# Optimization experiments

Measured on AMD Instinct MI355X. Metric: run time of the kernel, lower is better.

## Reference

```python
import jax, jax.numpy as jnp
import numpy as np

B, N_UNITS, SEQ, H = 4, 1024, 2048, 8
D_HEAD = N_UNITS // H
SCALE = 1.0 / D_HEAD ** 0.5


def setup_inputs() -> dict:
    key = jax.random.key(0)
    k1, k2, k3 = jax.random.split(key, 3)
    x = jax.random.normal(k1, (B, N_UNITS, SEQ), dtype=jnp.float32)
    # conv1x1 weights, bias=False; scaled like typical init
    W_qkv = jax.random.normal(k2, (3 * N_UNITS, N_UNITS), dtype=jnp.float32) * (1.0 / N_UNITS ** 0.5)
    W_out = jax.random.normal(k3, (N_UNITS, N_UNITS), dtype=jnp.float32) * (1.0 / N_UNITS ** 0.5)
    return {"x": x, "W_qkv": W_qkv, "W_out": W_out}


def reference(x, W_qkv, W_out):
    # x: (B, n_units, S). Conv1x1 == per-position linear along channel dim.
    qkv = jnp.einsum('oc,bcs->bos', W_qkv, x)          # (B, 3*n_units, S)
    Q, K, V = jnp.split(qkv, 3, axis=1)                # each (B, n_units, S)
    # torch.chunk along channels into h heads == reshape (B, h, d_head, S)
    Q = Q.reshape(B, H, D_HEAD, SEQ)
    K = K.reshape(B, H, D_HEAD, SEQ)
    V = V.reshape(B, H, D_HEAD, SEQ)
    # scores: Q^T K * scale  (NO softmax in original module; mask unused)
    A = jnp.einsum('bhdq,bhdk->bhqk', Q, K) * SCALE    # (B, h, S, S)
    # aggregation: sum_k A[q,k] * V[d,k]  (original does broadcast mul+sum)
    C = jnp.einsum('bhqk,bhdk->bhdq', A, V)            # (B, h, d_head, S)
    C = C.reshape(B, N_UNITS, SEQ)
    out = jnp.einsum('oc,bcs->bos', W_out, C)          # (B, n_units, S)
    return out
```

## Files before the change

kernel.cpp:

```cpp
#include <hip/hip_runtime.h>
#include <hip/hip_bf16.h>
#include <stdint.h>

using bf16 = __hip_bfloat16;

typedef __bf16 bf16x8 __attribute__((ext_vector_type(8)));
typedef float  f32x4  __attribute__((ext_vector_type(4)));

constexpr int Bc = 4, Hh = 8, Dh = 128, S = 2048, Cn = 1024, O3 = 3072;
constexpr float SCALE = 0.08838834764831845f;

#define GLDS16(gp, lp)                                               \
  __builtin_amdgcn_global_load_lds(                                  \
      (const __attribute__((address_space(1))) void*)(gp),           \
      (__attribute__((address_space(3))) void*)(lp), 16, 0, 0)

#define WAITVM(N) asm volatile("s_waitcnt vmcnt(" #N ")" ::: "memory")
#define BAR()                                  \
  do {                                         \
    asm volatile("" ::: "memory");             \
    __builtin_amdgcn_s_barrier();              \
    asm volatile("" ::: "memory");             \
  } while (0)

__device__ __forceinline__ void gemm_bt_core(
    const bf16* __restrict__ Abase, int lda,
    const bf16* __restrict__ Bbase, int ldb,
    int kIters, f32x4 (&acc)[4][4])
{
  alignas(16) __shared__ bf16 As[128 * 32];
  alignas(16) __shared__ bf16 Bs[128 * 32];
  const int t    = threadIdx.x;
  const int lane = t & 63;
  const int quad = lane >> 4, r16 = lane & 15;
  const int wave = t >> 6;
  const int wm = (wave & 1) * 64, wn = (wave >> 1) * 64;
  const int lrow = lane >> 2;
  const int lk   = (lane & 3) * 8;

  const long aOff0 = (long)(wave * 32 + lrow) * lda + lk;
  const long aOff1 = aOff0 + 16l * lda;
  const long bOff0 = (long)(wave * 32 + lrow) * ldb + lk;
  const long bOff1 = bOff0 + 16l * ldb;
  bf16* aL0 = &As[(wave * 32) * 32];
  bf16* aL1 = &As[(wave * 32 + 16) * 32];
  bf16* bL0 = &Bs[(wave * 32) * 32];
  bf16* bL1 = &Bs[(wave * 32 + 16) * 32];

#pragma unroll
  for (int i = 0; i < 4; i++)
#pragma unroll
    for (int j = 0; j < 4; j++) acc[i][j] = {0.f, 0.f, 0.f, 0.f};

  for (int ks = 0; ks < kIters; ++ks) {
    const int k0 = ks * 32;
    __syncthreads();
    GLDS16(Abase + k0 + aOff0, aL0);
    GLDS16(Abase + k0 + aOff1, aL1);
    GLDS16(Bbase + k0 + bOff0, bL0);
    GLDS16(Bbase + k0 + bOff1, bL1);
    __syncthreads();
    bf16x8 af[4], bfr[4];
#pragma unroll
    for (int i = 0; i < 4; i++)
      af[i] = *(const bf16x8*)&As[(wm + i * 16 + r16) * 32 + quad * 8];
#pragma unroll
    for (int j = 0; j < 4; j++)
      bfr[j] = *(const bf16x8*)&Bs[(wn + j * 16 + r16) * 32 + quad * 8];
#pragma unroll
    for (int i = 0; i < 4; i++)
#pragma unroll
      for (int j = 0; j < 4; j++)
        acc[i][j] = __builtin_amdgcn_mfma_f32_16x16x32_bf16(af[i], bfr[j], acc[i][j], 0, 0, 0);
  }
}

__device__ __forceinline__ void store_bf16_tile(
    f32x4 (&acc)[4][4], bf16* __restrict__ Cp, int ldc)
{
  const int t = threadIdx.x;
  const int lane = t & 63;
  const int quad = lane >> 4, r16 = lane & 15;
  const int wave = t >> 6;
  const int wm = (wave & 1) * 64, wn = (wave >> 1) * 64;
#pragma unroll
  for (int i = 0; i < 4; i++)
#pragma unroll
    for (int j = 0; j < 4; j++)
#pragma unroll
      for (int r = 0; r < 4; r++) {
        const int row = wm + i * 16 + quad * 4 + r;
        const int col = wn + j * 16 + r16;
        Cp[(long)row * ldc + col] = __float2bfloat16(acc[i][j][r]);
      }
}

__device__ __forceinline__ void store_f32_tile(
    f32x4 (&acc)[4][4], float* __restrict__ Cp, int ldc)
{
  const int t = threadIdx.x;
  const int lane = t & 63;
  const int quad = lane >> 4, r16 = lane & 15;
  const int wave = t >> 6;
  const int wm = (wave & 1) * 64, wn = (wave >> 1) * 64;
#pragma unroll
  for (int i = 0; i < 4; i++)
#pragma unroll
    for (int j = 0; j < 4; j++)
#pragma unroll
      for (int r = 0; r < 4; r++) {
        const int row = wm + i * 16 + quad * 4 + r;
        const int col = wn + j * 16 + r16;
        Cp[(long)row * ldc + col] = acc[i][j][r];
      }
}

__global__ __launch_bounds__(512, 2) void k_gemm_kv8(
    const bf16* __restrict__ WkvB, const bf16* __restrict__ xT, bf16* __restrict__ KV)
{
  constexpr int NT = Cn / 32;
  alignas(16) __shared__ bf16 smem[4 * 16384];

  const int orig = blockIdx.x;
  const int mt = orig >> 5;
  const int nt = ((orig & 7) << 2) | ((orig >> 3) & 3);
  const int m0 = mt * 256;

  const int tid  = threadIdx.x;
  const int lane = tid & 63;
  const int w    = tid >> 6;
  const int quad = lane >> 4, r16 = lane & 15;
  const int wm = (w >> 2) * 128;
  const int wn = (w & 3) * 64;

  const int srow = w * 16 + (lane >> 2);
  const int cx   = (lane & 3) ^ ((lane >> 3) & 3);
  const bf16* Ag = WkvB + (long)(m0 + srow) * Cn + cx * 8;
  const bf16* Bg = xT + (long)((long)nt * 256 + srow) * Cn + cx * 8;
  const int ldsW = w * 512;

#define KV8_STAGE_A(tt)                                                   \
  do {                                                                    \
    const int k0_ = (tt) * 32, bb_ = ((tt) & 3) * 16384;                  \
    GLDS16(Ag + k0_,             &smem[bb_ + ldsW]);                      \
    GLDS16(Ag + 128l * Cn + k0_, &smem[bb_ + 4096 + ldsW]);               \
  } while (0)
#define KV8_STAGE_B(tt)                                                   \
  do {                                                                    \
    const int k0_ = (tt) * 32, bb_ = ((tt) & 3) * 16384;                  \
    GLDS16(Bg + k0_,             &smem[bb_ + 8192 + ldsW]);               \
    GLDS16(Bg + 128l * Cn + k0_, &smem[bb_ + 8192 + 4096 + ldsW]);        \
  } while (0)

  const int sc8 = (quad ^ ((r16 >> 1) & 3)) * 8;

  f32x4 acc[8][4];
#pragma unroll
  for (int m = 0; m < 8; m++)
#pragma unroll
    for (int n = 0; n < 4; n++) acc[m][n] = {0.f, 0.f, 0.f, 0.f};

  KV8_STAGE_A(0); KV8_STAGE_B(0);
  KV8_STAGE_A(1); KV8_STAGE_B(1);
  KV8_STAGE_A(2); KV8_STAGE_B(2);
  WAITVM(8);
  BAR();

  bf16x8 af0[4], bfr0[4], af1[4];
  {
    const bf16* Ab = &smem[0];
    const bf16* Bb = Ab + 8192;
#pragma unroll
    for (int n = 0; n < 4; n++)
      bfr0[n] = *(const bf16x8*)&Bb[(wn + n * 16 + r16) * 32 + sc8];
#pragma unroll
    for (int m = 0; m < 4; m++)
      af0[m] = *(const bf16x8*)&Ab[(wm + m * 16 + r16) * 32 + sc8];
  }

#pragma unroll 4
  for (int tt = 0; tt < NT; ++tt) {
    const bf16* Ab = &smem[(tt & 3) * 16384];

    BAR();
    if (tt + 3 < NT) { KV8_STAGE_A(tt + 3); KV8_STAGE_B(tt + 3); }
#pragma unroll
    for (int m = 0; m < 4; m++)
      af1[m] = *(const bf16x8*)&Ab[(wm + (m + 4) * 16 + r16) * 32 + sc8];
    __builtin_amdgcn_s_setprio(1);
#pragma unroll
    for (int m = 0; m < 4; m++)
#pragma unroll
      for (int n = 0; n < 4; n++)
        acc[m][n] = __builtin_amdgcn_mfma_f32_16x16x32_bf16(af0[m], bfr0[n], acc[m][n], 0, 0, 0);
    __builtin_amdgcn_s_setprio(0);

    if (tt <= NT - 4)      { WAITVM(8); }
    else if (tt == NT - 3) { WAITVM(4); }
    else if (tt == NT - 2) { WAITVM(0); }
    BAR();

    __builtin_amdgcn_s_setprio(1);
#pragma unroll
    for (int m = 0; m < 4; m++)
#pragma unroll
      for (int n = 0; n < 4; n++)
        acc[m + 4][n] = __builtin_amdgcn_mfma_f32_16x16x32_bf16(af1[m], bfr0[n], acc[m + 4][n], 0, 0, 0);
    __builtin_amdgcn_s_setprio(0);

    if (tt + 1 < NT) {
      const bf16* Ab2 = &smem[((tt + 1) & 3) * 16384];
      const bf16* Bb2 = Ab2 + 8192;
#pragma unroll
      for (int n = 0; n < 4; n++)
        bfr0[n] = *(const bf16x8*)&Bb2[(wn + n * 16 + r16) * 32 + sc8];
#pragma unroll
      for (int m = 0; m < 4; m++)
        af0[m] = *(const bf16x8*)&Ab2[(wm + m * 16 + r16) * 32 + sc8];
    }
  }

  bf16* Cp = KV + (long)(nt >> 3) * 2048 * S + (long)m0 * S + (nt & 7) * 256;
#pragma unroll
  for (int m = 0; m < 8; m++)
#pragma unroll
    for (int n = 0; n < 4; n++)
#pragma unroll
      for (int r = 0; r < 4; r++) {
        const int row = wm + m * 16 + quad * 4 + r;
        const int col = wn + n * 16 + r16;
        Cp[(long)row * S + col] = __float2bfloat16(acc[m][n][r]);
      }
#undef KV8_STAGE_A
#undef KV8_STAGE_B
}

__global__ __launch_bounds__(512, 2) void k_gemm_out8(
    const bf16* __restrict__ W2, const bf16* __restrict__ QT, float* __restrict__ out)
{
  constexpr int NT = Cn / 32;
  alignas(16) __shared__ bf16 smem[4 * 12288];

  const int orig = blockIdx.x;
  const int swz  = (orig & 7) * 32 + (orig >> 3);
  const int b  = swz >> 6;
  const int mt = (swz >> 3) & 7;
  const int nt = swz & 7;
  const int m0 = mt * 128, n0 = nt * 256;

  const int tid  = threadIdx.x;
  const int lane = tid & 63;
  const int w    = tid >> 6;
  const int quad = lane >> 4, r16 = lane & 15;
  const int wm = (w >> 2) * 64;
  const int wn = (w & 3) * 64;

  const int srow = w * 16 + (lane >> 2);
  const int cx   = (lane & 3) ^ ((lane >> 3) & 3);
  const bf16* Ag = W2 + (long)b * Cn * Cn + (long)(m0 + srow) * Cn + cx * 8;
  const bf16* Bg = QT + (long)b * S * Cn + (long)(n0 + srow) * Cn + cx * 8;
  const int ldsW = w * 512;

#define OUT_STAGE(tt)                                                     \
  do {                                                                    \
    const int k0_ = (tt) * 32, bb_ = ((tt) & 3) * 12288;                  \
    GLDS16(Ag + k0_,             &smem[bb_ + ldsW]);                      \
    GLDS16(Bg + k0_,             &smem[bb_ + 4096 + ldsW]);               \
    GLDS16(Bg + 128l * Cn + k0_, &smem[bb_ + 8192 + ldsW]);               \
  } while (0)

  const int sc8 = (quad ^ ((r16 >> 1) & 3)) * 8;

  f32x4 acc[4][4];
#pragma unroll
  for (int m = 0; m < 4; m++)
#pragma unroll
    for (int n = 0; n < 4; n++) acc[m][n] = {0.f, 0.f, 0.f, 0.f};

  OUT_STAGE(0); OUT_STAGE(1); OUT_STAGE(2);
  WAITVM(6);
  BAR();

  bf16x8 af0[2], bfr0[4], af1[2];
  {
    const bf16* Ab = &smem[0];
    const bf16* Bb = Ab + 4096;
#pragma unroll
    for (int n = 0; n < 4; n++)
      bfr0[n] = *(const bf16x8*)&Bb[(wn + n * 16 + r16) * 32 + sc8];
#pragma unroll
    for (int m = 0; m < 2; m++)
      af0[m] = *(const bf16x8*)&Ab[(wm + m * 16 + r16) * 32 + sc8];
  }

#pragma unroll 4
  for (int tt = 0; tt < NT; ++tt) {
    const bf16* Ab = &smem[(tt & 3) * 12288];

    BAR();
    if (tt + 3 < NT) OUT_STAGE(tt + 3);
#pragma unroll
    for (int m = 0; m < 2; m++)
      af1[m] = *(const bf16x8*)&Ab[(wm + (m + 2) * 16 + r16) * 32 + sc8];
    __builtin_amdgcn_s_setprio(1);
#pragma unroll
    for (int m = 0; m < 2; m++)
#pragma unroll
      for (int n = 0; n < 4; n++)
        acc[m][n] = __builtin_amdgcn_mfma_f32_16x16x32_bf16(af0[m], bfr0[n], acc[m][n], 0, 0, 0);
    __builtin_amdgcn_s_setprio(0);

    if (tt <= NT - 4)      { WAITVM(6); }
    else if (tt == NT - 3) { WAITVM(3); }
    else if (tt == NT - 2) { WAITVM(0); }
    BAR();

    __builtin_amdgcn_s_setprio(1);
#pragma unroll
    for (int m = 0; m < 2; m++)
#pragma unroll
      for (int n = 0; n < 4; n++)
        acc[m + 2][n] = __builtin_amdgcn_mfma_f32_16x16x32_bf16(af1[m], bfr0[n], acc[m + 2][n], 0, 0, 0);
    __builtin_amdgcn_s_setprio(0);

    if (tt + 1 < NT) {
      const bf16* Ab2 = &smem[((tt + 1) & 3) * 12288];
      const bf16* Bb2 = Ab2 + 4096;
#pragma unroll
      for (int n = 0; n < 4; n++)
        bfr0[n] = *(const bf16x8*)&Bb2[(wn + n * 16 + r16) * 32 + sc8];
#pragma unroll
      for (int m = 0; m < 2; m++)
        af0[m] = *(const bf16x8*)&Ab2[(wm + m * 16 + r16) * 32 + sc8];
    }
  }

  float* Cp = out + (long)b * Cn * S + (long)m0 * S + n0;
#pragma unroll
  for (int m = 0; m < 4; m++)
#pragma unroll
    for (int n = 0; n < 4; n++)
#pragma unroll
      for (int r = 0; r < 4; r++) {
        const int row = wm + m * 16 + quad * 4 + r;
        const int col = wn + n * 16 + r16;
        Cp[(long)row * S + col] = acc[m][n][r];
      }
#undef OUT_STAGE
}

__global__ __launch_bounds__(512, 2) void k_gemm_qt8(
    const bf16* __restrict__ xT, const bf16* __restrict__ WqB, bf16* __restrict__ QT)
{
  constexpr int NT = Cn / 32;
  alignas(16) __shared__ bf16 smem[4 * 12288];

  const int orig = blockIdx.x;
  const int b  = orig >> 6;
  const int mt = (orig >> 2) & 15;
  const int nt = orig & 3;
  const int m0 = mt * 128, n0 = nt * 256;

  const int tid  = threadIdx.x;
  const int lane = tid & 63;
  const int w    = tid >> 6;
  const int quad = lane >> 4, r16 = lane & 15;
  const int wm = (w >> 2) * 64;
  const int wn = (w & 3) * 64;

  const int srow = w * 16 + (lane >> 2);
  const int cx   = (lane & 3) ^ ((lane >> 3) & 3);
  const bf16* Ag = xT + (long)b * S * Cn + (long)(m0 + srow) * Cn + cx * 8;
  const bf16* Bg = WqB + (long)(n0 + srow) * Cn + cx * 8;
  const int ldsW = w * 512;

#define QT_STAGE(tt)                                                      \
  do {                                                                    \
    const int k0_ = (tt) * 32, bb_ = ((tt) & 3) * 12288;                  \
    GLDS16(Ag + k0_,             &smem[bb_ + ldsW]);                      \
    GLDS16(Bg + k0_,             &smem[bb_ + 4096 + ldsW]);               \
    GLDS16(Bg + 128l * Cn + k0_, &smem[bb_ + 8192 + ldsW]);               \
  } while (0)

  const int sc8 = (quad ^ ((r16 >> 1) & 3)) * 8;

  f32x4 acc[4][4];
#pragma unroll
  for (int m = 0; m < 4; m++)
#pragma unroll
    for (int n = 0; n < 4; n++) acc[m][n] = {0.f, 0.f, 0.f, 0.f};

  QT_STAGE(0); QT_STAGE(1); QT_STAGE(2);
  WAITVM(6);
  BAR();

  bf16x8 af0[2], bfr0[4], af1[2];
  {
    const bf16* Ab = &smem[0];
    const bf16* Bb = Ab + 4096;
#pragma unroll
    for (int n = 0; n < 4; n++)
      bfr0[n] = *(const bf16x8*)&Bb[(wn + n * 16 + r16) * 32 + sc8];
#pragma unroll
    for (int m = 0; m < 2; m++)
      af0[m] = *(const bf16x8*)&Ab[(wm + m * 16 + r16) * 32 + sc8];
  }

#pragma unroll 4
  for (int tt = 0; tt < NT; ++tt) {
    const bf16* Ab = &smem[(tt & 3) * 12288];

    BAR();
    if (tt + 3 < NT) QT_STAGE(tt + 3);
#pragma unroll
    for (int m = 0; m < 2; m++)
      af1[m] = *(const bf16x8*)&Ab[(wm + (m + 2) * 16 + r16) * 32 + sc8];
    __builtin_amdgcn_s_setprio(1);
#pragma unroll
    for (int m = 0; m < 2; m++)
#pragma unroll
      for (int n = 0; n < 4; n++)
        acc[m][n] = __builtin_amdgcn_mfma_f32_16x16x32_bf16(af0[m], bfr0[n], acc[m][n], 0, 0, 0);
    __builtin_amdgcn_s_setprio(0);

    if (tt <= NT - 4)      { WAITVM(6); }
    else if (tt == NT - 3) { WAITVM(3); }
    else if (tt == NT - 2) { WAITVM(0); }
    BAR();

    __builtin_amdgcn_s_setprio(1);
#pragma unroll
    for (int m = 0; m < 2; m++)
#pragma unroll
      for (int n = 0; n < 4; n++)
        acc[m + 2][n] = __builtin_amdgcn_mfma_f32_16x16x32_bf16(af1[m], bfr0[n], acc[m + 2][n], 0, 0, 0);
    __builtin_amdgcn_s_setprio(0);

    if (tt + 1 < NT) {
      const bf16* Ab2 = &smem[((tt + 1) & 3) * 12288];
      const bf16* Bb2 = Ab2 + 4096;
#pragma unroll
      for (int n = 0; n < 4; n++)
        bfr0[n] = *(const bf16x8*)&Bb2[(wn + n * 16 + r16) * 32 + sc8];
#pragma unroll
      for (int m = 0; m < 2; m++)
        af0[m] = *(const bf16x8*)&Ab2[(wm + m * 16 + r16) * 32 + sc8];
    }
  }

  bf16* Cp = QT + (long)b * S * Cn + (long)m0 * Cn + n0;
#pragma unroll
  for (int m = 0; m < 4; m++)
#pragma unroll
    for (int n = 0; n < 4; n++)
#pragma unroll
      for (int r = 0; r < 4; r++) {
        const int row = wm + m * 16 + quad * 4 + r;
        const int col = wn + n * 16 + r16;
        Cp[(long)row * Cn + col] = __float2bfloat16(acc[m][n][r]);
      }
#undef QT_STAGE
}

__global__ __launch_bounds__(256) void k_cvt_w(
    const float* __restrict__ Wqkv, const float* __restrict__ Wout,
    bf16* __restrict__ WqkvB, bf16* __restrict__ WoutB)
{
  const long v = (long)blockIdx.x * 256 + threadIdx.x;
  const bool isQ = v < 786432;
  const float4 f = isQ ? ((const float4*)Wqkv)[v] : ((const float4*)Wout)[v - 786432];
  bf16 tmp[4];
  tmp[0] = __float2bfloat16(f.x);
  tmp[1] = __float2bfloat16(f.y);
  tmp[2] = __float2bfloat16(f.z);
  tmp[3] = __float2bfloat16(f.w);
  ushort4 u = *(ushort4*)tmp;
  if (isQ) ((ushort4*)WqkvB)[v] = u;
  else     ((ushort4*)WoutB)[v - 786432] = u;
}

__global__ __launch_bounds__(256) void k_transpose_cvt(
    const float* __restrict__ in, bf16* __restrict__ out, long inZ, long outZ)
{
  __shared__ bf16 tile[32][33];
  const float* ip = in + (long)blockIdx.z * inZ;
  bf16* op = out + (long)blockIdx.z * outZ;
  const int c0 = blockIdx.x * 32, r0 = blockIdx.y * 32;
  const int tx = threadIdx.x & 31, ty = threadIdx.x >> 5;
#pragma unroll
  for (int i = 0; i < 32; i += 8)
    tile[ty + i][tx] = __float2bfloat16(ip[(long)(r0 + ty + i) * 2048 + c0 + tx]);
  __syncthreads();
#pragma unroll
  for (int i = 0; i < 32; i += 8)
    op[(long)(c0 + ty + i) * 1024 + r0 + tx] = tile[tx][ty + i];
}

__global__ __launch_bounds__(256) void k_gemm_mt(
    const bf16* __restrict__ KV, float* __restrict__ MTpart)
{
  const int chunk = blockIdx.x;
  const int z = blockIdx.y;
  const int b = z >> 3, h = z & 7;
  const bf16* base = KV + (long)b * 2048 * S;
  const bf16* A  = base + (long)(h * Dh) * S + chunk * 256;
  const bf16* Bp = base + (long)(1024 + h * Dh) * S + chunk * 256;
  f32x4 acc[4][4];
  gemm_bt_core(A, S, Bp, S, 8, acc);
  store_f32_tile(acc, MTpart + ((long)chunk * 32 + z) * (Dh * Dh), Dh);
}

__global__ __launch_bounds__(256) void k_reduce_mt(
    const float* __restrict__ MTpart, bf16* __restrict__ MbT)
{
  const long i = (long)blockIdx.x * 256 + threadIdx.x;
  float s = 0.f;
#pragma unroll
  for (int c = 0; c < 8; c++) s += MTpart[(long)c * 32 * Dh * Dh + i];
  MbT[i] = __float2bfloat16(s * SCALE);
}

__global__ __launch_bounds__(256) void k_gemm_w2(
    const bf16* __restrict__ WoutB, const bf16* __restrict__ MbT, bf16* __restrict__ W2)
{
  const int m0 = blockIdx.x * 128;
  const int h = blockIdx.y, b = blockIdx.z;
  const int z = b * 8 + h;
  f32x4 acc[4][4];
  gemm_bt_core(WoutB + (long)m0 * Cn + h * Dh, Cn,
               MbT + (long)z * Dh * Dh, Dh, 4, acc);
  store_bf16_tile(acc, W2 + (long)b * Cn * Cn + (long)m0 * Cn + h * Dh, Cn);
}

extern "C" void kernel_launch(void* const* d_in, const int* in_sizes, int n_in,
                              void* d_out, int out_size, void* d_ws, size_t ws_size,
                              hipStream_t stream)
{
  const float* x    = (const float*)d_in[0];
  const float* Wqkv = (const float*)d_in[1];
  const float* Wout = (const float*)d_in[2];
  float* out = (float*)d_out;

  char* ws = (char*)d_ws;
  bf16*  KV     = (bf16*)ws;
  bf16*  xT     = (bf16*)(ws + 33554432);
  float* MTpart = (float*)(ws + 50331648);
  bf16*  QT     = (bf16*)(ws + 50331648);
  bf16*  WqkvB  = (bf16*)(ws + 67108864);
  bf16*  WoutB  = (bf16*)(ws + 73400320);
  bf16*  MbT    = (bf16*)(ws + 75497472);
  bf16*  W2     = (bf16*)(ws + 76546048);
  bf16*  WkvB   = WqkvB + (long)Cn * Cn;

  k_cvt_w<<<dim3(4096), 256, 0, stream>>>(Wqkv, Wout, WqkvB, WoutB);
  k_transpose_cvt<<<dim3(64, 32, 4), 256, 0, stream>>>(
      x, xT, (long)1024 * 2048, (long)2048 * 1024);
  k_gemm_kv8<<<dim3(256), 512, 0, stream>>>(WkvB, xT, KV);
  k_gemm_mt<<<dim3(8, 32), 256, 0, stream>>>(KV, MTpart);
  k_reduce_mt<<<dim3(2048), 256, 0, stream>>>(MTpart, MbT);
  k_gemm_w2<<<dim3(8, 8, 4), 256, 0, stream>>>(WoutB, MbT, W2);
  k_gemm_qt8<<<dim3(256), 512, 0, stream>>>(xT, WqkvB, QT);
  k_gemm_out8<<<dim3(256), 512, 0, stream>>>(W2, QT, out);
}
```

Baseline: 197.8 us.

## Merge KV and QT projection GEMMs into one launch and fuse prep kernels

The KV and Q^T projection GEMMs become device functions dispatched by block index inside one 512-block kernel, so both run concurrently and fill the GPU together. The weight conversion and the x transpose-convert kernels are merged into a single prep launch. MTpart scratch now lives in the output buffer, which is free until the final GEMM overwrites it. The cost is shared LDS sized for the larger KV body in both branches and a less balanced mix of block workloads.

```diff
diff --git a/kernel.cpp b/kernel.cpp
--- a/kernel.cpp
+++ b/kernel.cpp
@@ -115,13 +115,11 @@
       }
 }
 
-__global__ __launch_bounds__(512, 2) void k_gemm_kv8(
-    const bf16* __restrict__ WkvB, const bf16* __restrict__ xT, bf16* __restrict__ KV)
+__device__ __forceinline__ void kv_body(
+    const bf16* __restrict__ WkvB, const bf16* __restrict__ xT,
+    bf16* __restrict__ KV, bf16* sm, int orig)
 {
   constexpr int NT = Cn / 32;
-  alignas(16) __shared__ bf16 smem[4 * 16384];
-
-  const int orig = blockIdx.x;
   const int mt = orig >> 5;
   const int nt = ((orig & 7) << 2) | ((orig >> 3) & 3);
   const int m0 = mt * 256;
@@ -142,14 +140,14 @@
 #define KV8_STAGE_A(tt)                                                   \
   do {                                                                    \
     const int k0_ = (tt) * 32, bb_ = ((tt) & 3) * 16384;                  \
-    GLDS16(Ag + k0_,             &smem[bb_ + ldsW]);                      \
-    GLDS16(Ag + 128l * Cn + k0_, &smem[bb_ + 4096 + ldsW]);               \
+    GLDS16(Ag + k0_,             &sm[bb_ + ldsW]);                        \
+    GLDS16(Ag + 128l * Cn + k0_, &sm[bb_ + 4096 + ldsW]);                 \
   } while (0)
 #define KV8_STAGE_B(tt)                                                   \
   do {                                                                    \
     const int k0_ = (tt) * 32, bb_ = ((tt) & 3) * 16384;                  \
-    GLDS16(Bg + k0_,             &smem[bb_ + 8192 + ldsW]);               \
-    GLDS16(Bg + 128l * Cn + k0_, &smem[bb_ + 8192 + 4096 + ldsW]);        \
+    GLDS16(Bg + k0_,             &sm[bb_ + 8192 + ldsW]);                 \
+    GLDS16(Bg + 128l * Cn + k0_, &sm[bb_ + 8192 + 4096 + ldsW]);          \
   } while (0)
 
   const int sc8 = (quad ^ ((r16 >> 1) & 3)) * 8;
@@ -168,7 +166,7 @@
 
   bf16x8 af0[4], bfr0[4], af1[4];
   {
-    const bf16* Ab = &smem[0];
+    const bf16* Ab = &sm[0];
     const bf16* Bb = Ab + 8192;
 #pragma unroll
     for (int n = 0; n < 4; n++)
@@ -180,7 +178,7 @@
 
 #pragma unroll 4
   for (int tt = 0; tt < NT; ++tt) {
-    const bf16* Ab = &smem[(tt & 3) * 16384];
+    const bf16* Ab = &sm[(tt & 3) * 16384];
 
     BAR();
     if (tt + 3 < NT) { KV8_STAGE_A(tt + 3); KV8_STAGE_B(tt + 3); }
@@ -209,7 +207,7 @@
     __builtin_amdgcn_s_setprio(0);
 
     if (tt + 1 < NT) {
-      const bf16* Ab2 = &smem[((tt + 1) & 3) * 16384];
+      const bf16* Ab2 = &sm[((tt + 1) & 3) * 16384];
       const bf16* Bb2 = Ab2 + 8192;
 #pragma unroll
       for (int n = 0; n < 4; n++)
@@ -235,6 +233,164 @@
 #undef KV8_STAGE_B
 }
 
+__device__ __forceinline__ void qt_body(
+    const bf16* __restrict__ xT, const bf16* __restrict__ WqB,
+    bf16* __restrict__ QT, bf16* sm, int orig)
+{
+  constexpr int NT = Cn / 32;
+  const int b  = orig >> 6;
+  const int mt = (orig >> 2) & 15;
+  const int nt = orig & 3;
+  const int m0 = mt * 128, n0 = nt * 256;
+
+  const int tid  = threadIdx.x;
+  const int lane = tid & 63;
+  const int w    = tid >> 6;
+  const int quad = lane >> 4, r16 = lane & 15;
+  const int wm = (w >> 2) * 64;
+  const int wn = (w & 3) * 64;
+
+  const int srow = w * 16 + (lane >> 2);
+  const int cx   = (lane & 3) ^ ((lane >> 3) & 3);
+  const bf16* Ag = xT + (long)b * S * Cn + (long)(m0 + srow) * Cn + cx * 8;
+  const bf16* Bg = WqB + (long)(n0 + srow) * Cn + cx * 8;
+  const int ldsW = w * 512;
+
+#define QT_STAGE(tt)                                                      \
+  do {                                                                    \
+    const int k0_ = (tt) * 32, bb_ = ((tt) & 3) * 12288;                  \
+    GLDS16(Ag + k0_,             &sm[bb_ + ldsW]);                        \
+    GLDS16(Bg + k0_,             &sm[bb_ + 4096 + ldsW]);                 \
+    GLDS16(Bg + 128l * Cn + k0_, &sm[bb_ + 8192 + ldsW]);                 \
+  } while (0)
+
+  const int sc8 = (quad ^ ((r16 >> 1) & 3)) * 8;
+
+  f32x4 acc[4][4];
+#pragma unroll
+  for (int m = 0; m < 4; m++)
+#pragma unroll
+    for (int n = 0; n < 4; n++) acc[m][n] = {0.f, 0.f, 0.f, 0.f};
+
+  QT_STAGE(0); QT_STAGE(1); QT_STAGE(2);
+  WAITVM(6);
+  BAR();
+
+  bf16x8 af0[2], bfr0[4], af1[2];
+  {
+    const bf16* Ab = &sm[0];
+    const bf16* Bb = Ab + 4096;
+#pragma unroll
+    for (int n = 0; n < 4; n++)
+      bfr0[n] = *(const bf16x8*)&Bb[(wn + n * 16 + r16) * 32 + sc8];
+#pragma unroll
+    for (int m = 0; m < 2; m++)
+      af0[m] = *(const bf16x8*)&Ab[(wm + m * 16 + r16) * 32 + sc8];
+  }
+
+#pragma unroll 4
+  for (int tt = 0; tt < NT; ++tt) {
+    const bf16* Ab = &sm[(tt & 3) * 12288];
+
+    BAR();
+    if (tt + 3 < NT) QT_STAGE(tt + 3);
+#pragma unroll
+    for (int m = 0; m < 2; m++)
+      af1[m] = *(const bf16x8*)&Ab[(wm + (m + 2) * 16 + r16) * 32 + sc8];
+    __builtin_amdgcn_s_setprio(1);
+#pragma unroll
+    for (int m = 0; m < 2; m++)
+#pragma unroll
+      for (int n = 0; n < 4; n++)
+        acc[m][n] = __builtin_amdgcn_mfma_f32_16x16x32_bf16(af0[m], bfr0[n], acc[m][n], 0, 0, 0);
+    __builtin_amdgcn_s_setprio(0);
+
+    if (tt <= NT - 4)      { WAITVM(6); }
+    else if (tt == NT - 3) { WAITVM(3); }
+    else if (tt == NT - 2) { WAITVM(0); }
+    BAR();
+
+    __builtin_amdgcn_s_setprio(1);
+#pragma unroll
+    for (int m = 0; m < 2; m++)
+#pragma unroll
+      for (int n = 0; n < 4; n++)
+        acc[m + 2][n] = __builtin_amdgcn_mfma_f32_16x16x32_bf16(af1[m], bfr0[n], acc[m + 2][n], 0, 0, 0);
+    __builtin_amdgcn_s_setprio(0);
+
+    if (tt + 1 < NT) {
+      const bf16* Ab2 = &sm[((tt + 1) & 3) * 12288];
+      const bf16* Bb2 = Ab2 + 4096;
+#pragma unroll
+      for (int n = 0; n < 4; n++)
+        bfr0[n] = *(const bf16x8*)&Bb2[(wn + n * 16 + r16) * 32 + sc8];
+#pragma unroll
+      for (int m = 0; m < 2; m++)
+        af0[m] = *(const bf16x8*)&Ab2[(wm + m * 16 + r16) * 32 + sc8];
+    }
+  }
+
+  bf16* Cp = QT + (long)b * S * Cn + (long)m0 * Cn + n0;
+#pragma unroll
+  for (int m = 0; m < 4; m++)
+#pragma unroll
+    for (int n = 0; n < 4; n++)
+#pragma unroll
+      for (int r = 0; r < 4; r++) {
+        const int row = wm + m * 16 + quad * 4 + r;
+        const int col = wn + n * 16 + r16;
+        Cp[(long)row * Cn + col] = __float2bfloat16(acc[m][n][r]);
+      }
+#undef QT_STAGE
+}
+
+__global__ __launch_bounds__(512, 2) void k_kvqt8(
+    const bf16* __restrict__ WkvB, const bf16* __restrict__ xT,
+    bf16* __restrict__ KV, const bf16* __restrict__ WqB, bf16* __restrict__ QT)
+{
+  alignas(16) __shared__ bf16 smem[4 * 16384];
+  const int bid = blockIdx.x;
+  if (bid < 256) kv_body(WkvB, xT, KV, smem, bid);
+  else           qt_body(xT, WqB, QT, smem, bid - 256);
+}
+
+__global__ __launch_bounds__(256) void k_prep(
+    const float* __restrict__ x, bf16* __restrict__ xT,
+    const float* __restrict__ Wqkv, const float* __restrict__ Wout,
+    bf16* __restrict__ WqkvB, bf16* __restrict__ WoutB)
+{
+  __shared__ bf16 tile[32][33];
+  if (blockIdx.z < 4) {
+    const float* ip = x + (long)blockIdx.z * 1024 * 2048;
+    bf16* op = xT + (long)blockIdx.z * 2048 * 1024;
+    const int c0 = blockIdx.x * 32, r0 = blockIdx.y * 32;
+    const int tx = threadIdx.x & 31, ty = threadIdx.x >> 5;
+#pragma unroll
+    for (int i = 0; i < 32; i += 8)
+      tile[ty + i][tx] = __float2bfloat16(ip[(long)(r0 + ty + i) * 2048 + c0 + tx]);
+    __syncthreads();
+#pragma unroll
+    for (int i = 0; i < 32; i += 8)
+      op[(long)(c0 + ty + i) * 1024 + r0 + tx] = tile[tx][ty + i];
+  } else {
+    const long blk = (long)blockIdx.x + (long)blockIdx.y * 64;
+#pragma unroll
+    for (int i = 0; i < 2; i++) {
+      const long v = blk * 512 + i * 256 + threadIdx.x;
+      const bool isQ = v < 786432;
+      const float4 f = isQ ? ((const float4*)Wqkv)[v] : ((const float4*)Wout)[v - 786432];
+      bf16 tmp[4];
+      tmp[0] = __float2bfloat16(f.x);
+      tmp[1] = __float2bfloat16(f.y);
+      tmp[2] = __float2bfloat16(f.z);
+      tmp[3] = __float2bfloat16(f.w);
+      ushort4 u = *(ushort4*)tmp;
+      if (isQ) ((ushort4*)WqkvB)[v] = u;
+      else     ((ushort4*)WoutB)[v - 786432] = u;
+    }
+  }
+}
+
 __global__ __launch_bounds__(512, 2) void k_gemm_out8(
     const bf16* __restrict__ W2, const bf16* __restrict__ QT, float* __restrict__ out)
 {
@@ -347,153 +503,6 @@
         Cp[(long)row * S + col] = acc[m][n][r];
       }
 #undef OUT_STAGE
-}
-
-__global__ __launch_bounds__(512, 2) void k_gemm_qt8(
-    const bf16* __restrict__ xT, const bf16* __restrict__ WqB, bf16* __restrict__ QT)
-{
-  constexpr int NT = Cn / 32;
-  alignas(16) __shared__ bf16 smem[4 * 12288];
-
-  const int orig = blockIdx.x;
-  const int b  = orig >> 6;
-  const int mt = (orig >> 2) & 15;
-  const int nt = orig & 3;
-  const int m0 = mt * 128, n0 = nt * 256;
-
-  const int tid  = threadIdx.x;
-  const int lane = tid & 63;
-  const int w    = tid >> 6;
-  const int quad = lane >> 4, r16 = lane & 15;
-  const int wm = (w >> 2) * 64;
-  const int wn = (w & 3) * 64;
-
-  const int srow = w * 16 + (lane >> 2);
-  const int cx   = (lane & 3) ^ ((lane >> 3) & 3);
-  const bf16* Ag = xT + (long)b * S * Cn + (long)(m0 + srow) * Cn + cx * 8;
-  const bf16* Bg = WqB + (long)(n0 + srow) * Cn + cx * 8;
-  const int ldsW = w * 512;
-
-#define QT_STAGE(tt)                                                      \
-  do {                                                                    \
-    const int k0_ = (tt) * 32, bb_ = ((tt) & 3) * 12288;                  \
-    GLDS16(Ag + k0_,             &smem[bb_ + ldsW]);                      \
-    GLDS16(Bg + k0_,             &smem[bb_ + 4096 + ldsW]);               \
-    GLDS16(Bg + 128l * Cn + k0_, &smem[bb_ + 8192 + ldsW]);               \
-  } while (0)
-
-  const int sc8 = (quad ^ ((r16 >> 1) & 3)) * 8;
-
-  f32x4 acc[4][4];
-#pragma unroll
-  for (int m = 0; m < 4; m++)
-#pragma unroll
-    for (int n = 0; n < 4; n++) acc[m][n] = {0.f, 0.f, 0.f, 0.f};
-
-  QT_STAGE(0); QT_STAGE(1); QT_STAGE(2);
-  WAITVM(6);
-  BAR();
-
-  bf16x8 af0[2], bfr0[4], af1[2];
-  {
-    const bf16* Ab = &smem[0];
-    const bf16* Bb = Ab + 4096;
-#pragma unroll
-    for (int n = 0; n < 4; n++)
-      bfr0[n] = *(const bf16x8*)&Bb[(wn + n * 16 + r16) * 32 + sc8];
-#pragma unroll
-    for (int m = 0; m < 2; m++)
-      af0[m] = *(const bf16x8*)&Ab[(wm + m * 16 + r16) * 32 + sc8];
-  }
-
-#pragma unroll 4
-  for (int tt = 0; tt < NT; ++tt) {
-    const bf16* Ab = &smem[(tt & 3) * 12288];
-
-    BAR();
-    if (tt + 3 < NT) QT_STAGE(tt + 3);
-#pragma unroll
-    for (int m = 0; m < 2; m++)
-      af1[m] = *(const bf16x8*)&Ab[(wm + (m + 2) * 16 + r16) * 32 + sc8];
-    __builtin_amdgcn_s_setprio(1);
-#pragma unroll
-    for (int m = 0; m < 2; m++)
-#pragma unroll
-      for (int n = 0; n < 4; n++)
-        acc[m][n] = __builtin_amdgcn_mfma_f32_16x16x32_bf16(af0[m], bfr0[n], acc[m][n], 0, 0, 0);
-    __builtin_amdgcn_s_setprio(0);
-
-    if (tt <= NT - 4)      { WAITVM(6); }
-    else if (tt == NT - 3) { WAITVM(3); }
-    else if (tt == NT - 2) { WAITVM(0); }
-    BAR();
-
-    __builtin_amdgcn_s_setprio(1);
-#pragma unroll
-    for (int m = 0; m < 2; m++)
-#pragma unroll
-      for (int n = 0; n < 4; n++)
-        acc[m + 2][n] = __builtin_amdgcn_mfma_f32_16x16x32_bf16(af1[m], bfr0[n], acc[m + 2][n], 0, 0, 0);
-    __builtin_amdgcn_s_setprio(0);
-
-    if (tt + 1 < NT) {
-      const bf16* Ab2 = &smem[((tt + 1) & 3) * 12288];
-      const bf16* Bb2 = Ab2 + 4096;
-#pragma unroll
-      for (int n = 0; n < 4; n++)
-        bfr0[n] = *(const bf16x8*)&Bb2[(wn + n * 16 + r16) * 32 + sc8];
-#pragma unroll
-      for (int m = 0; m < 2; m++)
-        af0[m] = *(const bf16x8*)&Ab2[(wm + m * 16 + r16) * 32 + sc8];
-    }
-  }
-
-  bf16* Cp = QT + (long)b * S * Cn + (long)m0 * Cn + n0;
-#pragma unroll
-  for (int m = 0; m < 4; m++)
-#pragma unroll
-    for (int n = 0; n < 4; n++)
-#pragma unroll
-      for (int r = 0; r < 4; r++) {
-        const int row = wm + m * 16 + quad * 4 + r;
-        const int col = wn + n * 16 + r16;
-        Cp[(long)row * Cn + col] = __float2bfloat16(acc[m][n][r]);
-      }
-#undef QT_STAGE
-}
-
-__global__ __launch_bounds__(256) void k_cvt_w(
-    const float* __restrict__ Wqkv, const float* __restrict__ Wout,
-    bf16* __restrict__ WqkvB, bf16* __restrict__ WoutB)
-{
-  const long v = (long)blockIdx.x * 256 + threadIdx.x;
-  const bool isQ = v < 786432;
-  const float4 f = isQ ? ((const float4*)Wqkv)[v] : ((const float4*)Wout)[v - 786432];
-  bf16 tmp[4];
-  tmp[0] = __float2bfloat16(f.x);
-  tmp[1] = __float2bfloat16(f.y);
-  tmp[2] = __float2bfloat16(f.z);
-  tmp[3] = __float2bfloat16(f.w);
-  ushort4 u = *(ushort4*)tmp;
-  if (isQ) ((ushort4*)WqkvB)[v] = u;
-  else     ((ushort4*)WoutB)[v - 786432] = u;
-}
-
-__global__ __launch_bounds__(256) void k_transpose_cvt(
-    const float* __restrict__ in, bf16* __restrict__ out, long inZ, long outZ)
-{
-  __shared__ bf16 tile[32][33];
-  const float* ip = in + (long)blockIdx.z * inZ;
-  bf16* op = out + (long)blockIdx.z * outZ;
-  const int c0 = blockIdx.x * 32, r0 = blockIdx.y * 32;
-  const int tx = threadIdx.x & 31, ty = threadIdx.x >> 5;
-#pragma unroll
-  for (int i = 0; i < 32; i += 8)
-    tile[ty + i][tx] = __float2bfloat16(ip[(long)(r0 + ty + i) * 2048 + c0 + tx]);
-  __syncthreads();
-#pragma unroll
-  for (int i = 0; i < 32; i += 8)
-    op[(long)(c0 + ty + i) * 1024 + r0 + tx] = tile[tx][ty + i];
 }
 
 __global__ __launch_bounds__(256) void k_gemm_mt(
@@ -544,21 +553,18 @@
   char* ws = (char*)d_ws;
   bf16*  KV     = (bf16*)ws;
   bf16*  xT     = (bf16*)(ws + 33554432);
-  float* MTpart = (float*)(ws + 50331648);
   bf16*  QT     = (bf16*)(ws + 50331648);
   bf16*  WqkvB  = (bf16*)(ws + 67108864);
   bf16*  WoutB  = (bf16*)(ws + 73400320);
   bf16*  MbT    = (bf16*)(ws + 75497472);
   bf16*  W2     = (bf16*)(ws + 76546048);
   bf16*  WkvB   = WqkvB + (long)Cn * Cn;
-
-  k_cvt_w<<<dim3(4096), 256, 0, stream>>>(Wqkv, Wout, WqkvB, WoutB);
-  k_transpose_cvt<<<dim3(64, 32, 4), 256, 0, stream>>>(
-      x, xT, (long)1024 * 2048, (long)2048 * 1024);
-  k_gemm_kv8<<<dim3(256), 512, 0, stream>>>(WkvB, xT, KV);
+  float* MTpart = out;
+
+  k_prep<<<dim3(64, 32, 5), 256, 0, stream>>>(x, xT, Wqkv, Wout, WqkvB, WoutB);
+  k_kvqt8<<<dim3(512), 512, 0, stream>>>(WkvB, xT, KV, WqkvB, QT);
   k_gemm_mt<<<dim3(8, 32), 256, 0, stream>>>(KV, MTpart);
   k_reduce_mt<<<dim3(2048), 256, 0, stream>>>(MTpart, MbT);
   k_gemm_w2<<<dim3(8, 8, 4), 256, 0, stream>>>(WoutB, MbT, W2);
-  k_gemm_qt8<<<dim3(256), 512, 0, stream>>>(xT, WqkvB, QT);
   k_gemm_out8<<<dim3(256), 512, 0, stream>>>(W2, QT, out);
 }
```

New measurement: 198.0 us. No clear change (+0.1%).
